# Performance work log

Hardware: AMD Instinct MI355X
Metric: run time of the kernel (lower is better)

The kernel has to match this reference:

```python
import jax, jax.numpy as jnp
import numpy as np


def setup_inputs() -> dict:
    key = jax.random.key(0)
    k1, k2, k3 = jax.random.split(key, 3)
    num, c_in, c_out, nx, ny, din, dout = 128, 3, 8, 31, 31, 4, 6
    x = jax.random.normal(k1, (num, c_in, din, nx + 1, ny + 1), dtype=jnp.float32)
    tensors = jax.random.normal(k2, (c_in, c_out, nx, ny, din, din, din, din, dout), dtype=jnp.float32)
    bias = jax.random.normal(k3, (c_out, nx, ny, dout), dtype=jnp.float32) * 1e-8
    return {"x": x, "tensors": tensors, "bias": bias}


def reference(x, tensors, bias):
    # x: [num, c_in, din, sx, sy]; tensors: [c_in, c_out, nx, ny, din,din,din,din, dout]
    num, c_in, din, sx, sy = x.shape
    X, Y = sx - 1, sy - 1  # == nx, ny
    c_out, dout = tensors.shape[1], tensors.shape[-1]
    # four 2x2-patch corners, each [num, c_in, din, X, Y]
    a = x[:, :, :, :-1, :-1]
    b = x[:, :, :, 1:, :-1]
    c = x[:, :, :, :-1, 1:]
    d = x[:, :, :, 1:, 1:]
    # outer product of the four corner vectors -> rank-4 local feature [num, c_in, din^4, X, Y]
    ab = jnp.einsum('ncixy,ncjxy->ncijxy', a, b)
    cd = jnp.einsum('nckxy,nclxy->ncklxy', c, d)
    patch = jnp.einsum('ncijxy,ncklxy->ncijklxy', ab, cd)
    patch = patch.reshape(num, c_in, din ** 4, X, Y)
    # per-position weight: [c_in, c_out, X, Y, din^4, dout]
    w = tensors.reshape(c_in, c_out, X, Y, din ** 4, dout)
    out = jnp.einsum('ncmxy,cpxymo->npoxy', patch, w)  # [num, c_out, dout, X, Y]
    out = out + bias.transpose(0, 3, 1, 2)[None]  # bias -> [1, c_out, dout, X, Y]
    return out
```

## Files before the change

kernel.cpp:

```cpp
#include <hip/hip_runtime.h>


typedef __attribute__((ext_vector_type(8))) short short8;
typedef __attribute__((ext_vector_type(4))) float floatx4;
typedef __attribute__((ext_vector_type(4))) unsigned int uintx4;

#define WS_ELEMS (961u * 6144u)
#define SA_STR 72
#define SW_STR 72

static __device__ __forceinline__ unsigned short f2bf(float f) {
  union { float f; unsigned u; } v; v.f = f;
  unsigned r = v.u + 0x7FFFu + ((v.u >> 16) & 1u);
  return (unsigned short)(r >> 16);
}

static __device__ __forceinline__ void barrier_lgkm() {
  asm volatile("s_waitcnt lgkmcnt(0)\n\ts_barrier" ::: "memory");
  __builtin_amdgcn_sched_barrier(0);
}

template <bool TO_WS>
__global__ __launch_bounds__(256, 4)
void ttn_conv_mfma(const float* __restrict__ x,
                   const float* __restrict__ tensors,
                   const float* __restrict__ bias,
                   float* __restrict__ dst) {
  __shared__ __align__(16) unsigned short sA[128 * SA_STR];
  __shared__ __align__(16) unsigned short sW[48 * SW_STR];

  const int site = blockIdx.x;
  const int xx = site / 31, yy = site - xx * 31;
  const int t = threadIdx.x;
  const int lane = t & 63, wave = t >> 6;
  const int row = lane & 15, quad = lane >> 4;

  const int n_st = t & 127;
  const int h = t >> 7;
  const int p_st = t >> 5;
  const int q_st = t & 31;

  floatx4 acc[2][3];
#pragma unroll
  for (int i0 = 0; i0 < 2; ++i0)
#pragma unroll
    for (int j0 = 0; j0 < 3; ++j0)
      acc[i0][j0] = (floatx4){0.f, 0.f, 0.f, 0.f};

  float areg[4], b0 = 0.f, b1 = 0.f, cdreg[16];
  float4 wv[12];

#pragma unroll
  for (int ch = 0; ch < 12; ++ch) {
    const int mb = ch & 3;
    if ((ch & 3) == 0) {
      const int c = ch >> 2;
      const float* xp = x + ((size_t)n_st * 3 + c) * 4096 + xx * 32 + yy;
      float bq[4], cq[4], dq[4];
#pragma unroll
      for (int i = 0; i < 4; ++i) {
        const float* r0 = xp + i * 1024;
        areg[i] = r0[0];
        cq[i]   = r0[1];
        bq[i]   = r0[32];
        dq[i]   = r0[33];
      }
      {
        const float* src =
            tensors + ((size_t)((c * 8 + p_st) * 961 + site)) * 1536 + 12 * q_st;
#pragma unroll
        for (int mb2 = 0; mb2 < 4; ++mb2) {
          wv[3 * mb2 + 0] = *(const float4*)(src + mb2 * 384);
          wv[3 * mb2 + 1] = *(const float4*)(src + mb2 * 384 + 4);
          wv[3 * mb2 + 2] = *(const float4*)(src + mb2 * 384 + 8);
        }
      }
      b0 = h ? bq[2] : bq[0];
      b1 = h ? bq[3] : bq[1];
#pragma unroll
      for (int k2 = 0; k2 < 4; ++k2)
#pragma unroll
        for (int l2 = 0; l2 < 4; ++l2)
          cdreg[k2 * 4 + l2] = cq[k2] * dq[l2];
    }
    barrier_lgkm();

#pragma unroll
    for (int e = 0; e < 2; ++e) {
      const float ab = areg[mb] * (e ? b1 : b0);
      unsigned pk[8];
#pragma unroll
      for (int u = 0; u < 8; ++u)
        pk[u] = (unsigned)f2bf(ab * cdreg[2 * u]) |
                ((unsigned)f2bf(ab * cdreg[2 * u + 1]) << 16);
      uintx4* dp = (uintx4*)&sA[n_st * SA_STR + (2 * h + e) * 16];
      uintx4 v0 = {pk[0], pk[1], pk[2], pk[3]};
      uintx4 v1 = {pk[4], pk[5], pk[6], pk[7]};
      dp[0] = v0;
      dp[1] = v1;
    }
    {
      const float4 w0 = wv[3 * mb + 0];
      const float4 w1 = wv[3 * mb + 1];
      const float4 w2 = wv[3 * mb + 2];
      unsigned short* dW = &sW[(p_st * 6) * SW_STR + 2 * q_st];
      *(unsigned*)&dW[0 * SW_STR] = (unsigned)f2bf(w0.x) | ((unsigned)f2bf(w1.z) << 16);
      *(unsigned*)&dW[1 * SW_STR] = (unsigned)f2bf(w0.y) | ((unsigned)f2bf(w1.w) << 16);
      *(unsigned*)&dW[2 * SW_STR] = (unsigned)f2bf(w0.z) | ((unsigned)f2bf(w2.x) << 16);
      *(unsigned*)&dW[3 * SW_STR] = (unsigned)f2bf(w0.w) | ((unsigned)f2bf(w2.y) << 16);
      *(unsigned*)&dW[4 * SW_STR] = (unsigned)f2bf(w1.x) | ((unsigned)f2bf(w2.z) << 16);
      *(unsigned*)&dW[5 * SW_STR] = (unsigned)f2bf(w1.y) | ((unsigned)f2bf(w2.w) << 16);
    }
    barrier_lgkm();

#pragma unroll
    for (int ks = 0; ks < 2; ++ks) {
      const int kof = ks * 32 + quad * 8;
      short8 af[2], bf[3];
#pragma unroll
      for (int mt = 0; mt < 2; ++mt)
        af[mt] = *(const short8*)&sA[(wave * 32 + mt * 16 + row) * SA_STR + kof];
#pragma unroll
      for (int nt = 0; nt < 3; ++nt)
        bf[nt] = *(const short8*)&sW[(nt * 16 + row) * SW_STR + kof];
#pragma unroll
      for (int mt = 0; mt < 2; ++mt)
#pragma unroll
        for (int nt = 0; nt < 3; ++nt)
          acc[mt][nt] = __builtin_amdgcn_mfma_f32_16x16x32_bf16(
              af[mt], bf[nt], acc[mt][nt], 0, 0, 0);
    }
  }

  if (TO_WS) {
#pragma unroll
    for (int mt = 0; mt < 2; ++mt)
#pragma unroll
      for (int r = 0; r < 4; ++r) {
        const int n = wave * 32 + mt * 16 + quad * 4 + r;
#pragma unroll
        for (int nt = 0; nt < 3; ++nt) {
          const int po = nt * 16 + row;
          dst[(size_t)site * 6144 + n * 48 + po] = acc[mt][nt][r];
        }
      }
  } else {
#pragma unroll
    for (int mt = 0; mt < 2; ++mt)
#pragma unroll
      for (int r = 0; r < 4; ++r) {
        const int n = wave * 32 + mt * 16 + quad * 4 + r;
#pragma unroll
        for (int nt = 0; nt < 3; ++nt) {
          const int po = nt * 16 + row;
          const int p = po / 6, o = po - p * 6;
          dst[(size_t)(n * 48 + po) * 961 + site] =
              acc[mt][nt][r] + bias[(p * 961 + site) * 6 + o];
        }
      }
  }
}

__global__ __launch_bounds__(256, 8)
void ttn_transpose_bias(const float* __restrict__ ws,
                        const float* __restrict__ bias,
                        float* __restrict__ out) {
  __shared__ float tile[32][33];
  const int f0 = blockIdx.x * 32;
  const int s0 = blockIdx.y * 32;
  const int tx = threadIdx.x;
  const int ty = threadIdx.y;

#pragma unroll
  for (int rr = 0; rr < 4; ++rr) {
    const int srow = ty + rr * 8;
    const int site = s0 + srow;
    if (site < 961)
      tile[srow][tx] = ws[(size_t)site * 6144 + f0 + tx];
  }
  __syncthreads();

#pragma unroll
  for (int rr = 0; rr < 4; ++rr) {
    const int fy = ty + rr * 8;
    const int f = f0 + fy;
    const int site = s0 + tx;
    if (site < 961) {
      const int po = f % 48;
      const int p = po / 6, o = po - p * 6;
      out[(size_t)f * 961 + site] = tile[tx][fy] + bias[(p * 961 + site) * 6 + o];
    }
  }
}

extern "C" void kernel_launch(void* const* d_in, const int* in_sizes, int n_in,
                              void* d_out, int out_size, void* d_ws, size_t ws_size,
                              hipStream_t stream) {
  const float* x       = (const float*)d_in[0];
  const float* tensors = (const float*)d_in[1];
  const float* bias    = (const float*)d_in[2];
  float* out           = (float*)d_out;

  const size_t need = (size_t)WS_ELEMS * sizeof(float);
  if (d_ws != nullptr && ws_size >= need) {
    float* ws = (float*)d_ws;
    hipLaunchKernelGGL((ttn_conv_mfma<true>), dim3(961), dim3(256), 0, stream,
                       x, tensors, bias, ws);
    hipLaunchKernelGGL(ttn_transpose_bias, dim3(192, 31), dim3(32, 8), 0, stream,
                       ws, bias, out);
  } else {
    hipLaunchKernelGGL((ttn_conv_mfma<false>), dim3(961), dim3(256), 0, stream,
                       x, tensors, bias, out);
  }
}
```

Baseline: 250.2 us.

## Double-buffer LDS tiles and prefetch next channel's inputs and weights

The conv kernel now uses two LDS buffers for the patch and weight tiles, so building the next k-chunk overlaps with the MFMA work on the current one, and it needs only one barrier per chunk. Global loads for the next input channel's x corners and weights are issued early, ahead of their use. Occupancy hint drops from 4 to 3 blocks per CU to make room for the extra LDS and registers. The cost is higher register and LDS pressure, which may reduce wave-level latency hiding.

```diff
diff --git a/kernel.cpp b/kernel.cpp
--- a/kernel.cpp
+++ b/kernel.cpp
@@ -21,13 +21,13 @@
 }
 
 template <bool TO_WS>
-__global__ __launch_bounds__(256, 4)
+__global__ __launch_bounds__(256, 3)
 void ttn_conv_mfma(const float* __restrict__ x,
                    const float* __restrict__ tensors,
                    const float* __restrict__ bias,
                    float* __restrict__ dst) {
-  __shared__ __align__(16) unsigned short sA[128 * SA_STR];
-  __shared__ __align__(16) unsigned short sW[48 * SW_STR];
+  __shared__ __align__(16) unsigned short sA[2][128 * SA_STR];
+  __shared__ __align__(16) unsigned short sW[2][48 * SW_STR];
 
   const int site = blockIdx.x;
   const int xx = site / 31, yy = site - xx * 31;
@@ -48,62 +48,109 @@
       acc[i0][j0] = (floatx4){0.f, 0.f, 0.f, 0.f};
 
   float areg[4], b0 = 0.f, b1 = 0.f, cdreg[16];
+  float nxa[4], nxb[4], nxc[4], nxd[4];
   float4 wv[12];
 
-#pragma unroll
-  for (int ch = 0; ch < 12; ++ch) {
-    const int mb = ch & 3;
-    if ((ch & 3) == 0) {
-      const int c = ch >> 2;
-      const float* xp = x + ((size_t)n_st * 3 + c) * 4096 + xx * 32 + yy;
-      float bq[4], cq[4], dq[4];
-#pragma unroll
-      for (int i = 0; i < 4; ++i) {
-        const float* r0 = xp + i * 1024;
-        areg[i] = r0[0];
-        cq[i]   = r0[1];
-        bq[i]   = r0[32];
-        dq[i]   = r0[33];
-      }
-      {
-        const float* src =
-            tensors + ((size_t)((c * 8 + p_st) * 961 + site)) * 1536 + 12 * q_st;
-#pragma unroll
-        for (int mb2 = 0; mb2 < 4; ++mb2) {
-          wv[3 * mb2 + 0] = *(const float4*)(src + mb2 * 384);
-          wv[3 * mb2 + 1] = *(const float4*)(src + mb2 * 384 + 4);
-          wv[3 * mb2 + 2] = *(const float4*)(src + mb2 * 384 + 8);
-        }
-      }
-      b0 = h ? bq[2] : bq[0];
-      b1 = h ? bq[3] : bq[1];
-#pragma unroll
-      for (int k2 = 0; k2 < 4; ++k2)
-#pragma unroll
-        for (int l2 = 0; l2 < 4; ++l2)
-          cdreg[k2 * 4 + l2] = cq[k2] * dq[l2];
-    }
-    barrier_lgkm();
-
+  const float* xbase = x + (size_t)n_st * 3 * 4096 + xx * 32 + yy;
+  const float* wsite = tensors + ((size_t)(p_st * 961 + site)) * 1536 + 12 * q_st;
+
+  {
+    float bq[4], cq[4], dq[4];
+#pragma unroll
+    for (int i = 0; i < 4; ++i) {
+      const float* r0 = xbase + i * 1024;
+      areg[i] = r0[0];
+      cq[i]   = r0[1];
+      bq[i]   = r0[32];
+      dq[i]   = r0[33];
+    }
+    b0 = h ? bq[2] : bq[0];
+    b1 = h ? bq[3] : bq[1];
+#pragma unroll
+    for (int k2 = 0; k2 < 4; ++k2)
+#pragma unroll
+      for (int l2 = 0; l2 < 4; ++l2)
+        cdreg[k2 * 4 + l2] = cq[k2] * dq[l2];
+  }
+#pragma unroll
+  for (int mb2 = 0; mb2 < 4; ++mb2) {
+    wv[3 * mb2 + 0] = *(const float4*)(wsite + mb2 * 384);
+    wv[3 * mb2 + 1] = *(const float4*)(wsite + mb2 * 384 + 4);
+    wv[3 * mb2 + 2] = *(const float4*)(wsite + mb2 * 384 + 8);
+  }
+  {
 #pragma unroll
     for (int e = 0; e < 2; ++e) {
-      const float ab = areg[mb] * (e ? b1 : b0);
+      const float ab = areg[0] * (e ? b1 : b0);
       unsigned pk[8];
 #pragma unroll
       for (int u = 0; u < 8; ++u)
         pk[u] = (unsigned)f2bf(ab * cdreg[2 * u]) |
                 ((unsigned)f2bf(ab * cdreg[2 * u + 1]) << 16);
-      uintx4* dp = (uintx4*)&sA[n_st * SA_STR + (2 * h + e) * 16];
+      uintx4* dp = (uintx4*)&sA[0][n_st * SA_STR + (2 * h + e) * 16];
       uintx4 v0 = {pk[0], pk[1], pk[2], pk[3]};
       uintx4 v1 = {pk[4], pk[5], pk[6], pk[7]};
       dp[0] = v0;
       dp[1] = v1;
     }
-    {
-      const float4 w0 = wv[3 * mb + 0];
-      const float4 w1 = wv[3 * mb + 1];
-      const float4 w2 = wv[3 * mb + 2];
-      unsigned short* dW = &sW[(p_st * 6) * SW_STR + 2 * q_st];
+    const float4 w0 = wv[0], w1 = wv[1], w2 = wv[2];
+    unsigned short* dW = &sW[0][(p_st * 6) * SW_STR + 2 * q_st];
+    *(unsigned*)&dW[0 * SW_STR] = (unsigned)f2bf(w0.x) | ((unsigned)f2bf(w1.z) << 16);
+    *(unsigned*)&dW[1 * SW_STR] = (unsigned)f2bf(w0.y) | ((unsigned)f2bf(w1.w) << 16);
+    *(unsigned*)&dW[2 * SW_STR] = (unsigned)f2bf(w0.z) | ((unsigned)f2bf(w2.x) << 16);
+    *(unsigned*)&dW[3 * SW_STR] = (unsigned)f2bf(w0.w) | ((unsigned)f2bf(w2.y) << 16);
+    *(unsigned*)&dW[4 * SW_STR] = (unsigned)f2bf(w1.x) | ((unsigned)f2bf(w2.z) << 16);
+    *(unsigned*)&dW[5 * SW_STR] = (unsigned)f2bf(w1.y) | ((unsigned)f2bf(w2.w) << 16);
+  }
+
+#pragma unroll
+  for (int ch = 0; ch < 12; ++ch) {
+    barrier_lgkm();
+
+    if ((ch & 3) == 0 && (ch >> 2) < 2) {
+      const int cn = (ch >> 2) + 1;
+      const float* xp = xbase + cn * 4096;
+#pragma unroll
+      for (int i = 0; i < 4; ++i) {
+        const float* r0 = xp + i * 1024;
+        nxa[i] = r0[0];
+        nxc[i] = r0[1];
+        nxb[i] = r0[32];
+        nxd[i] = r0[33];
+      }
+    }
+    if ((ch & 3) == 3 && (ch >> 2) < 2) {
+#pragma unroll
+      for (int i = 0; i < 4; ++i) areg[i] = nxa[i];
+      b0 = h ? nxb[2] : nxb[0];
+      b1 = h ? nxb[3] : nxb[1];
+#pragma unroll
+      for (int k2 = 0; k2 < 4; ++k2)
+#pragma unroll
+        for (int l2 = 0; l2 < 4; ++l2)
+          cdreg[k2 * 4 + l2] = nxc[k2] * nxd[l2];
+    }
+    if (ch < 11) {
+      const int mb1 = (ch + 1) & 3;
+      const int bs = (ch + 1) & 1;
+#pragma unroll
+      for (int e = 0; e < 2; ++e) {
+        const float ab = areg[mb1] * (e ? b1 : b0);
+        unsigned pk[8];
+#pragma unroll
+        for (int u = 0; u < 8; ++u)
+          pk[u] = (unsigned)f2bf(ab * cdreg[2 * u]) |
+                  ((unsigned)f2bf(ab * cdreg[2 * u + 1]) << 16);
+        uintx4* dp = (uintx4*)&sA[bs][n_st * SA_STR + (2 * h + e) * 16];
+        uintx4 v0 = {pk[0], pk[1], pk[2], pk[3]};
+        uintx4 v1 = {pk[4], pk[5], pk[6], pk[7]};
+        dp[0] = v0;
+        dp[1] = v1;
+      }
+      const float4 w0 = wv[3 * mb1 + 0];
+      const float4 w1 = wv[3 * mb1 + 1];
+      const float4 w2 = wv[3 * mb1 + 2];
+      unsigned short* dW = &sW[bs][(p_st * 6) * SW_STR + 2 * q_st];
       *(unsigned*)&dW[0 * SW_STR] = (unsigned)f2bf(w0.x) | ((unsigned)f2bf(w1.z) << 16);
       *(unsigned*)&dW[1 * SW_STR] = (unsigned)f2bf(w0.y) | ((unsigned)f2bf(w1.w) << 16);
       *(unsigned*)&dW[2 * SW_STR] = (unsigned)f2bf(w0.z) | ((unsigned)f2bf(w2.x) << 16);
@@ -111,7 +158,16 @@
       *(unsigned*)&dW[4 * SW_STR] = (unsigned)f2bf(w1.x) | ((unsigned)f2bf(w2.z) << 16);
       *(unsigned*)&dW[5 * SW_STR] = (unsigned)f2bf(w1.y) | ((unsigned)f2bf(w2.w) << 16);
     }
-    barrier_lgkm();
+    if ((ch & 3) == 2 && (ch >> 2) < 2) {
+      const int cn = (ch >> 2) + 1;
+      const float* src = wsite + (size_t)cn * 8 * 961 * 1536;
+#pragma unroll
+      for (int mb2 = 0; mb2 < 4; ++mb2) {
+        wv[3 * mb2 + 0] = *(const float4*)(src + mb2 * 384);
+        wv[3 * mb2 + 1] = *(const float4*)(src + mb2 * 384 + 4);
+        wv[3 * mb2 + 2] = *(const float4*)(src + mb2 * 384 + 8);
+      }
+    }
 
 #pragma unroll
     for (int ks = 0; ks < 2; ++ks) {
@@ -119,10 +175,10 @@
       short8 af[2], bf[3];
 #pragma unroll
       for (int mt = 0; mt < 2; ++mt)
-        af[mt] = *(const short8*)&sA[(wave * 32 + mt * 16 + row) * SA_STR + kof];
+        af[mt] = *(const short8*)&sA[ch & 1][(wave * 32 + mt * 16 + row) * SA_STR + kof];
 #pragma unroll
       for (int nt = 0; nt < 3; ++nt)
-        bf[nt] = *(const short8*)&sW[(nt * 16 + row) * SW_STR + kof];
+        bf[nt] = *(const short8*)&sW[ch & 1][(nt * 16 + row) * SW_STR + kof];
 #pragma unroll
       for (int mt = 0; mt < 2; ++mt)
 #pragma unroll
```

New measurement: 244.6 us. 1.02x faster.
